# Optimization experiments

Measured on AMD Instinct MI355X. Metric: run time of the kernel, lower is better.

## Reference

```python
import jax, jax.numpy as jnp
import numpy as np

D_MODEL = 1024
NUM_HEADS = 16
D_K = D_MODEL // NUM_HEADS


def setup_inputs() -> dict:
    key = jax.random.key(0)
    ks = jax.random.split(key, 11)
    B, S = 4, 2048
    s = 1.0 / np.sqrt(D_MODEL)
    inp = {
        "q": jax.random.normal(ks[0], (B, S, D_MODEL), jnp.float32),
        "k": jax.random.normal(ks[1], (B, S, D_MODEL), jnp.float32),
        "v": jax.random.normal(ks[2], (B, S, D_MODEL), jnp.float32),
        "w_q": jax.random.normal(ks[3], (D_MODEL, D_MODEL), jnp.float32) * s,
        "b_q": jnp.zeros((D_MODEL,), jnp.float32),
        "w_k": jax.random.normal(ks[4], (D_MODEL, D_MODEL), jnp.float32) * s,
        "b_k": jnp.zeros((D_MODEL,), jnp.float32),
        "w_v": jax.random.normal(ks[5], (D_MODEL, D_MODEL), jnp.float32) * s,
        "b_v": jnp.zeros((D_MODEL,), jnp.float32),
        "w_o": jax.random.normal(ks[6], (D_MODEL, D_MODEL), jnp.float32) * s,
        "b_o": jnp.zeros((D_MODEL,), jnp.float32),
    }
    return inp


def reference(q, k, v, w_q, b_q, w_k, b_k, w_v, b_v, w_o, b_o):
    B, S, _ = q.shape
    # projections; weights stored as [in, out] so x @ W + b
    def proj(x, w, b):
        y = x @ w + b  # [B, S, d_model]
        return y.reshape(B, -1, NUM_HEADS, D_K).transpose(0, 2, 1, 3)  # [B,H,S,d_k]
    qh = proj(q, w_q, b_q)
    kh = proj(k, w_k, b_k)
    vh = proj(v, w_v, b_v)
    scores = jnp.einsum("bhsd,bhtd->bhst", qh, kh) / jnp.sqrt(jnp.float32(D_K))
    attn = jax.nn.softmax(scores, axis=-1)  # dropout p=0.0 -> identity
    x = jnp.einsum("bhst,bhtd->bhsd", attn, vh)
    x = x.transpose(0, 2, 1, 3).reshape(B, S, D_MODEL)
    return x @ w_o + b_o
```

## Files before the change

kernel.cpp:

```cpp
#include <hip/hip_runtime.h>
#include <hip/hip_bf16.h>
#include <stdint.h>

#define D_MODEL 1024
#define SEQ 2048
#define BATCH 4
#define NHEADS 16
#define ROWS (BATCH*SEQ)

#define QKSCALE 0.18033688011f

typedef __attribute__((ext_vector_type(4))) float f32x4;
typedef __attribute__((ext_vector_type(8))) short short8;
typedef __attribute__((ext_vector_type(4))) unsigned int uint4v;

#if __has_builtin(__builtin_amdgcn_exp2f)
#define EXP2(x) __builtin_amdgcn_exp2f(x)
#else
#define EXP2(x) exp2f(x)
#endif

__device__ __forceinline__ unsigned short f2bf(float f) {
    unsigned int x = __builtin_bit_cast(unsigned int, f);
    x += 0x7fffu + ((x >> 16) & 1u);
    return (unsigned short)(x >> 16);
}

__device__ __forceinline__ unsigned int cvtpk(float a, float b) {
    unsigned int r;
    asm("v_cvt_pk_bf16_f32 %0, %1, %2" : "=v"(r) : "v"(a), "v"(b));
    return r;
}

__global__ __launch_bounds__(256) void wtrans_kernel(const float* __restrict__ w0,
                                                     const float* __restrict__ w1,
                                                     const float* __restrict__ w2,
                                                     const float* __restrict__ w3,
                                                     unsigned short* __restrict__ wt0,
                                                     unsigned short* __restrict__ wt1,
                                                     unsigned short* __restrict__ wt2,
                                                     unsigned short* __restrict__ wt3) {
    const int z = blockIdx.z;
    const float* w = (z == 0) ? w0 : (z == 1) ? w1 : (z == 2) ? w2 : w3;
    unsigned short* wt = (z == 0) ? wt0 : (z == 1) ? wt1 : (z == 2) ? wt2 : wt3;
    __shared__ float tile[32][33];
    int tx = threadIdx.x & 31;
    int ty = threadIdx.x >> 5;
    int r0 = blockIdx.y * 32, c0 = blockIdx.x * 32;
    #pragma unroll
    for (int i = 0; i < 4; ++i)
        tile[ty + 8*i][tx] = w[(size_t)(r0 + ty + 8*i) * D_MODEL + (c0 + tx)];
    __syncthreads();
    int t = threadIdx.x;
    if (t < 128) {
        int n_loc = t >> 2;
        int kc = t & 3;
        int n = c0 + n_loc;
        int kbase = r0 + kc*8;
        uint4v pk;
        #pragma unroll
        for (int j = 0; j < 4; ++j)
            pk[j] = cvtpk(tile[kc*8 + 2*j][n_loc], tile[kc*8 + 2*j + 1][n_loc]);
        size_t tidx = (size_t)(n >> 7) * 16 + (kbase >> 6);
        int row = n & 127;
        int byte = (row*128 + (kbase & 63)*2) ^ ((row & 7) << 4);
        *(uint4v*)((char*)wt + tidx*16384 + byte) = pk;
    }
}

__global__ __launch_bounds__(256) void qkv_gemm_kernel(
        const float* __restrict__ qin, const float* __restrict__ kin,
        const float* __restrict__ vin,
        const unsigned short* __restrict__ wqt, const unsigned short* __restrict__ wkt,
        const unsigned short* __restrict__ wvt,
        const float* __restrict__ bq, const float* __restrict__ bk,
        const float* __restrict__ bv,
        unsigned short* __restrict__ qhd, unsigned short* __restrict__ khd,
        unsigned short* __restrict__ vtd) {
    __shared__ __attribute__((aligned(16))) unsigned short Alds[2][128*64];
    __shared__ __attribute__((aligned(16))) unsigned short Blds[2][128*64];
    const int z = blockIdx.z;
    const float* Af = (z == 0) ? qin : (z == 1) ? kin : vin;
    const unsigned short* Bt = (z == 0) ? wqt : (z == 1) ? wkt : wvt;
    const float* bias = (z == 0) ? bq : (z == 1) ? bk : bv;
    const int m0 = blockIdx.x * 128;
    const int n0 = blockIdx.y * 128;
    const int t = threadIdx.x;
    const int lane = t & 63;
    const int w = t >> 6;
    const int wm = w >> 1, wn = w & 1;
    const int l15 = lane & 15, lg = lane >> 4;

    f32x4 acc[4][4];
    #pragma unroll
    for (int i = 0; i < 4; ++i)
        #pragma unroll
        for (int j = 0; j < 4; ++j) acc[i][j] = (f32x4)(0.0f);

    #pragma unroll
    for (int i = 0; i < 8; ++i) {
        int idx = t + i*256;
        int row = idx >> 4, c4 = idx & 15;
        f32x4 v = *(const f32x4*)(Af + (size_t)(m0+row)*D_MODEL + c4*4);
        unsigned long long pk = (unsigned long long)cvtpk(v[0], v[1])
                              | ((unsigned long long)cvtpk(v[2], v[3]) << 32);
        int byte = (row*128 + c4*8) ^ ((row & 7) << 4);
        *(unsigned long long*)((char*)Alds[0] + byte) = pk;
    }
    {
        const unsigned short* tsrc = Bt + (size_t)(n0 >> 7) * 16 * 8192;
        #pragma unroll
        for (int i = 0; i < 4; ++i)
            __builtin_amdgcn_global_load_lds(
                (const __attribute__((address_space(1))) void*)(tsrc + t*8 + i*2048),
                (__attribute__((address_space(3))) void*)(Blds[0] + t*8 + i*2048),
                16, 0, 0);
    }
    __syncthreads();

    #pragma unroll 2
    for (int kt = 0; kt < 16; ++kt) {
        const int cur = kt & 1, nxt = cur ^ 1;
        const int k0n = (kt + 1) * 64;
        f32x4 av[8];
        if (kt < 15) {
            #pragma unroll
            for (int i = 0; i < 8; ++i) {
                int idx = t + i*256;
                int row = idx >> 4, c4 = idx & 15;
                av[i] = *(const f32x4*)(Af + (size_t)(m0+row)*D_MODEL + k0n + c4*4);
            }
            const unsigned short* tsrc = Bt + ((size_t)(n0 >> 7) * 16 + (k0n >> 6)) * 8192;
            #pragma unroll
            for (int i = 0; i < 4; ++i)
                __builtin_amdgcn_global_load_lds(
                    (const __attribute__((address_space(1))) void*)(tsrc + t*8 + i*2048),
                    (__attribute__((address_space(3))) void*)(Blds[nxt] + t*8 + i*2048),
                    16, 0, 0);
        }

        #pragma unroll
        for (int kk = 0; kk < 2; ++kk) {
            short8 af[4], bfr[4];
            #pragma unroll
            for (int mi = 0; mi < 4; ++mi) {
                int row = wm*64 + mi*16 + l15;
                int byte = (row*128 + kk*64 + lg*16) ^ ((row & 7) << 4);
                af[mi] = *(const short8*)((const char*)Alds[cur] + byte);
            }
            #pragma unroll
            for (int ni = 0; ni < 4; ++ni) {
                int row = wn*64 + ni*16 + l15;
                int byte = (row*128 + kk*64 + lg*16) ^ ((row & 7) << 4);
                bfr[ni] = *(const short8*)((const char*)Blds[cur] + byte);
            }
            #pragma unroll
            for (int mi = 0; mi < 4; ++mi)
                #pragma unroll
                for (int ni = 0; ni < 4; ++ni)
                    acc[mi][ni] = __builtin_amdgcn_mfma_f32_16x16x32_bf16(
                        af[mi], bfr[ni], acc[mi][ni], 0, 0, 0);
        }

        if (kt < 15) {
            #pragma unroll
            for (int i = 0; i < 8; ++i) {
                int idx = t + i*256;
                int row = idx >> 4, c4 = idx & 15;
                unsigned long long pk = (unsigned long long)cvtpk(av[i][0], av[i][1])
                                      | ((unsigned long long)cvtpk(av[i][2], av[i][3]) << 32);
                int byte = (row*128 + c4*8) ^ ((row & 7) << 4);
                *(unsigned long long*)((char*)Alds[nxt] + byte) = pk;
            }
        }
        __syncthreads();
    }

    #pragma unroll
    for (int mi = 0; mi < 4; ++mi)
        #pragma unroll
        for (int ni = 0; ni < 4; ++ni) {
            int col = n0 + wn*64 + ni*16 + l15;
            float bv_ = bias[col];
            int h = col >> 6, d = col & 63;
            if (z == 0) {
                #pragma unroll
                for (int r = 0; r < 4; ++r) {
                    int row = m0 + wm*64 + mi*16 + lg*4 + r;
                    int bb = row >> 11, s = row & 2047;
                    float vv = (acc[mi][ni][r] + bv_) * QKSCALE;
                    qhd[(((size_t)(bb*NHEADS + h)*SEQ + s) << 6) + d] = f2bf(vv);
                }
            } else if (z == 1) {
                #pragma unroll
                for (int r = 0; r < 4; ++r) {
                    int row = m0 + wm*64 + mi*16 + lg*4 + r;
                    int bb = row >> 11, s = row & 2047;
                    int ti = s >> 6, kvl = s & 63;
                    int ph = (kvl & 0x23) | ((kvl & 4) << 2) | ((kvl & 0x18) >> 1);
                    int byte = (ph*128 + d*2) ^ ((ph & 7) << 4);
                    *(unsigned short*)((char*)khd
                        + ((size_t)(bb*NHEADS + h)*32 + ti)*8192 + byte)
                        = f2bf(acc[mi][ni][r] + bv_);
                }
            } else {
                int row0 = m0 + wm*64 + mi*16 + lg*4;
                int bb = row0 >> 11, s0 = row0 & 2047;
                int ti = s0 >> 6, kvl0 = s0 & 63;
                unsigned long long pk = 0;
                #pragma unroll
                for (int r = 0; r < 4; ++r)
                    pk |= (unsigned long long)f2bf(acc[mi][ni][r] + bv_) << (16*r);
                int byte = (d*128 + kvl0*2) ^ ((d & 7) << 4);
                *(unsigned long long*)((char*)vtd
                    + ((size_t)(bb*NHEADS + h)*32 + ti)*8192 + byte) = pk;
            }
        }
}

__global__ __launch_bounds__(256) void out_gemm_kernel(const unsigned short* __restrict__ Ab,
                                                       const unsigned short* __restrict__ Bt,
                                                       const float* __restrict__ bias,
                                                       float* __restrict__ Out) {
    __shared__ __attribute__((aligned(16))) unsigned short Alds[2][128*64];
    __shared__ __attribute__((aligned(16))) unsigned short Blds[2][128*64];
    const int m0 = blockIdx.x * 128;
    const int n0 = blockIdx.y * 128;
    const int t = threadIdx.x;
    const int lane = t & 63;
    const int w = t >> 6;
    const int wm = w >> 1, wn = w & 1;
    const int l15 = lane & 15, lg = lane >> 4;

    const int arow = t >> 3;
    const int acb = ((t & 7) * 16) ^ ((arow & 7) << 4);

    f32x4 acc[4][4];
    #pragma unroll
    for (int i = 0; i < 4; ++i)
        #pragma unroll
        for (int j = 0; j < 4; ++j) acc[i][j] = (f32x4)(0.0f);

    #pragma unroll
    for (int i = 0; i < 4; ++i) {
        const char* src = (const char*)(Ab + (size_t)(m0 + arow + i*32)*D_MODEL) + acb;
        __builtin_amdgcn_global_load_lds(
            (const __attribute__((address_space(1))) void*)src,
            (__attribute__((address_space(3))) void*)(Alds[0] + t*8 + i*2048),
            16, 0, 0);
    }
    {
        const unsigned short* tsrc = Bt + (size_t)(n0 >> 7) * 16 * 8192;
        #pragma unroll
        for (int i = 0; i < 4; ++i)
            __builtin_amdgcn_global_load_lds(
                (const __attribute__((address_space(1))) void*)(tsrc + t*8 + i*2048),
                (__attribute__((address_space(3))) void*)(Blds[0] + t*8 + i*2048),
                16, 0, 0);
    }
    __syncthreads();

    #pragma unroll 2
    for (int kt = 0; kt < 16; ++kt) {
        const int cur = kt & 1, nxt = cur ^ 1;
        const int k0n = (kt + 1) * 64;
        if (kt < 15) {
            #pragma unroll
            for (int i = 0; i < 4; ++i) {
                const char* src = (const char*)(Ab + (size_t)(m0 + arow + i*32)*D_MODEL + k0n) + acb;
                __builtin_amdgcn_global_load_lds(
                    (const __attribute__((address_space(1))) void*)src,
                    (__attribute__((address_space(3))) void*)(Alds[nxt] + t*8 + i*2048),
                    16, 0, 0);
            }
            const unsigned short* tsrc = Bt + ((size_t)(n0 >> 7) * 16 + (k0n >> 6)) * 8192;
            #pragma unroll
            for (int i = 0; i < 4; ++i)
                __builtin_amdgcn_global_load_lds(
                    (const __attribute__((address_space(1))) void*)(tsrc + t*8 + i*2048),
                    (__attribute__((address_space(3))) void*)(Blds[nxt] + t*8 + i*2048),
                    16, 0, 0);
        }

        #pragma unroll
        for (int kk = 0; kk < 2; ++kk) {
            short8 af[4], bfr[4];
            #pragma unroll
            for (int mi = 0; mi < 4; ++mi) {
                int row = wm*64 + mi*16 + l15;
                int byte = (row*128 + kk*64 + lg*16) ^ ((row & 7) << 4);
                af[mi] = *(const short8*)((const char*)Alds[cur] + byte);
            }
            #pragma unroll
            for (int ni = 0; ni < 4; ++ni) {
                int row = wn*64 + ni*16 + l15;
                int byte = (row*128 + kk*64 + lg*16) ^ ((row & 7) << 4);
                bfr[ni] = *(const short8*)((const char*)Blds[cur] + byte);
            }
            #pragma unroll
            for (int mi = 0; mi < 4; ++mi)
                #pragma unroll
                for (int ni = 0; ni < 4; ++ni)
                    acc[mi][ni] = __builtin_amdgcn_mfma_f32_16x16x32_bf16(
                        af[mi], bfr[ni], acc[mi][ni], 0, 0, 0);
        }
        __syncthreads();
    }

    #pragma unroll
    for (int mi = 0; mi < 4; ++mi)
        #pragma unroll
        for (int ni = 0; ni < 4; ++ni) {
            int col = n0 + wn*64 + ni*16 + l15;
            float bv_ = bias[col];
            #pragma unroll
            for (int r = 0; r < 4; ++r) {
                int row = m0 + wm*64 + mi*16 + lg*4 + r;
                Out[(size_t)row*D_MODEL + col] = acc[mi][ni][r] + bv_;
            }
        }
}

__global__ __launch_bounds__(256, 4) void attn_kernel(const unsigned short* __restrict__ qh,
                                                      const unsigned short* __restrict__ kimg_all,
                                                      const unsigned short* __restrict__ vimg_all,
                                                      unsigned short* __restrict__ xout) {
    __shared__ __attribute__((aligned(16))) unsigned short Klds[2][64*64];
    __shared__ __attribute__((aligned(16))) unsigned short Vtl[2][64*64];

    const int bid = blockIdx.x;
    const int xcd = bid & 7, idx = bid >> 3;
    const int qb = idx >> 3;
    const int bh = ((idx & 7) << 3) | xcd;
    const int t = threadIdx.x;
    const int lane = t & 63;
    const int w = t >> 6;
    const int l15 = lane & 15, lg = lane >> 4;

    const unsigned short* qbase = qh + (size_t)bh * SEQ * 64;
    const unsigned short* kimg = kimg_all + (size_t)bh * SEQ * 64;
    const unsigned short* vimg = vimg_all + (size_t)bh * SEQ * 64;

    short8 qf[2][2];
    #pragma unroll
    for (int l = 0; l < 2; ++l) {
        int qrow = qb*128 + w*32 + l*16 + l15;
        qf[l][0] = *(const short8*)(qbase + (size_t)qrow*64 + lg*8);
        qf[l][1] = *(const short8*)(qbase + (size_t)qrow*64 + 32 + lg*8);
    }

    int fb[4][2];
    #pragma unroll
    for (int nb = 0; nb < 4; ++nb) {
        int rr = nb*16 + l15;
        int sw = (rr & 7) << 4;
        fb[nb][0] = (rr*128 + lg*16) ^ sw;
        fb[nb][1] = (rr*128 + 64 + lg*16) ^ sw;
    }

    float m[2] = {-1e30f, -1e30f};
    float lsum[2] = {0.f, 0.f};
    f32x4 o[2][4];
    #pragma unroll
    for (int l = 0; l < 2; ++l)
        #pragma unroll
        for (int nb = 0; nb < 4; ++nb) o[l][nb] = (f32x4)(0.0f);

    #pragma unroll
    for (int i = 0; i < 2; ++i) {
        __builtin_amdgcn_global_load_lds(
            (const __attribute__((address_space(1))) void*)(kimg + t*8 + i*2048),
            (__attribute__((address_space(3))) void*)(Klds[0] + t*8 + i*2048), 16, 0, 0);
        __builtin_amdgcn_global_load_lds(
            (const __attribute__((address_space(1))) void*)(vimg + t*8 + i*2048),
            (__attribute__((address_space(3))) void*)(Vtl[0] + t*8 + i*2048), 16, 0, 0);
    }
    __syncthreads();

    const unsigned short* kp = kimg + 4096 + t*8;
    const unsigned short* vp = vimg + 4096 + t*8;

    const int NT = SEQ/64;
    #pragma unroll 2
    for (int ti = 0; ti < NT; ++ti) {
        const int c = ti & 1;
        if (ti + 1 < NT) {
            #pragma unroll
            for (int i = 0; i < 2; ++i) {
                __builtin_amdgcn_global_load_lds(
                    (const __attribute__((address_space(1))) void*)(kp + i*2048),
                    (__attribute__((address_space(3))) void*)(Klds[c^1] + t*8 + i*2048), 16, 0, 0);
                __builtin_amdgcn_global_load_lds(
                    (const __attribute__((address_space(1))) void*)(vp + i*2048),
                    (__attribute__((address_space(3))) void*)(Vtl[c^1] + t*8 + i*2048), 16, 0, 0);
            }
            kp += 4096; vp += 4096;
        }
        const char* Kc = (const char*)Klds[c];
        const char* Vc = (const char*)Vtl[c];

        f32x4 s4[2][4];
        #pragma unroll
        for (int nb = 0; nb < 4; ++nb) {
            short8 kf0 = *(const short8*)(Kc + fb[nb][0]);
            short8 kf1 = *(const short8*)(Kc + fb[nb][1]);
            __builtin_amdgcn_s_setprio(1);
            #pragma unroll
            for (int l = 0; l < 2; ++l) {
                f32x4 s = (f32x4)(0.0f);
                s = __builtin_amdgcn_mfma_f32_16x16x32_bf16(kf0, qf[l][0], s, 0, 0, 0);
                s = __builtin_amdgcn_mfma_f32_16x16x32_bf16(kf1, qf[l][1], s, 0, 0, 0);
                s4[l][nb] = s;
            }
            __builtin_amdgcn_s_setprio(0);
        }

        if (ti == 0) {
            #pragma unroll
            for (int l = 0; l < 2; ++l) {
                float tm = s4[l][0][0];
                #pragma unroll
                for (int nb = 0; nb < 4; ++nb)
                    #pragma unroll
                    for (int r = 0; r < 4; ++r) tm = fmaxf(tm, s4[l][nb][r]);
                tm = fmaxf(tm, __shfl_xor(tm, 16));
                tm = fmaxf(tm, __shfl_xor(tm, 32));
                m[l] = tm;
            }
        }

        union U { short8 s; unsigned int u[4]; } pa[2][2];
        #pragma unroll
        for (int l = 0; l < 2; ++l) {
            float p[16];
            float ts = 0.f;
            #pragma unroll
            for (int nb = 0; nb < 4; ++nb)
                #pragma unroll
                for (int r = 0; r < 4; ++r) {
                    float pv = EXP2(s4[l][nb][r] - m[l]);
                    p[nb*4 + r] = pv;
                    ts += pv;
                }
            lsum[l] += ts;

            pa[l][0].u[0] = cvtpk(p[0],  p[1]);  pa[l][0].u[1] = cvtpk(p[2],  p[3]);
            pa[l][0].u[2] = cvtpk(p[4],  p[5]);  pa[l][0].u[3] = cvtpk(p[6],  p[7]);
            pa[l][1].u[0] = cvtpk(p[8],  p[9]);  pa[l][1].u[1] = cvtpk(p[10], p[11]);
            pa[l][1].u[2] = cvtpk(p[12], p[13]); pa[l][1].u[3] = cvtpk(p[14], p[15]);
        }

        #pragma unroll
        for (int nb = 0; nb < 4; ++nb) {
            short8 vf0 = *(const short8*)(Vc + fb[nb][0]);
            short8 vf1 = *(const short8*)(Vc + fb[nb][1]);
            __builtin_amdgcn_s_setprio(1);
            o[0][nb] = __builtin_amdgcn_mfma_f32_16x16x32_bf16(pa[0][0].s, vf0, o[0][nb], 0, 0, 0);
            o[0][nb] = __builtin_amdgcn_mfma_f32_16x16x32_bf16(pa[0][1].s, vf1, o[0][nb], 0, 0, 0);
            o[1][nb] = __builtin_amdgcn_mfma_f32_16x16x32_bf16(pa[1][0].s, vf0, o[1][nb], 0, 0, 0);
            o[1][nb] = __builtin_amdgcn_mfma_f32_16x16x32_bf16(pa[1][1].s, vf1, o[1][nb], 0, 0, 0);
            __builtin_amdgcn_s_setprio(0);
        }

        __syncthreads();
    }

    const int bb = bh >> 4, h = bh & 15;
    #pragma unroll
    for (int l = 0; l < 2; ++l) {
        float lt = lsum[l];
        lt += __shfl_xor(lt, 16);
        lt += __shfl_xor(lt, 32);
        float rl[4];
        #pragma unroll
        for (int r = 0; r < 4; ++r) rl[r] = 1.0f / __shfl(lt, lg*4 + r);
        #pragma unroll
        for (int nb = 0; nb < 4; ++nb)
            #pragma unroll
            for (int r = 0; r < 4; ++r) {
                int s = qb*128 + w*32 + l*16 + lg*4 + r;
                int d = nb*16 + l15;
                xout[((size_t)(bb*SEQ + s))*D_MODEL + h*64 + d] = f2bf(o[l][nb][r] * rl[r]);
            }
    }
}

extern "C" void kernel_launch(void* const* d_in, const int* in_sizes, int n_in,
                              void* d_out, int out_size, void* d_ws, size_t ws_size,
                              hipStream_t stream) {
    (void)in_sizes; (void)n_in; (void)out_size; (void)ws_size;
    const float* q  = (const float*)d_in[0];
    const float* k  = (const float*)d_in[1];
    const float* v  = (const float*)d_in[2];
    const float* wq = (const float*)d_in[3];
    const float* bq = (const float*)d_in[4];
    const float* wk = (const float*)d_in[5];
    const float* bk = (const float*)d_in[6];
    const float* wv = (const float*)d_in[7];
    const float* bv = (const float*)d_in[8];
    const float* wo = (const float*)d_in[9];
    const float* bo = (const float*)d_in[10];

    char* ws = (char*)d_ws;
    unsigned short* wqt = (unsigned short*)(ws);
    unsigned short* wkt = (unsigned short*)(ws + (2ull << 20));
    unsigned short* wvt = (unsigned short*)(ws + (4ull << 20));
    unsigned short* wot = (unsigned short*)(ws + (6ull << 20));
    unsigned short* qhd = (unsigned short*)(ws + (8ull << 20));
    unsigned short* khd = (unsigned short*)(ws + (24ull << 20));
    unsigned short* vtd = (unsigned short*)(ws + (40ull << 20));
    unsigned short* xat = (unsigned short*)(ws + (56ull << 20));

    hipLaunchKernelGGL(wtrans_kernel, dim3(D_MODEL/32, D_MODEL/32, 4), dim3(256), 0, stream,
                       wq, wk, wv, wo, wqt, wkt, wvt, wot);

    hipLaunchKernelGGL(qkv_gemm_kernel, dim3(ROWS/128, D_MODEL/128, 3), dim3(256), 0, stream,
                       q, k, v, wqt, wkt, wvt, bq, bk, bv, qhd, khd, vtd);

    hipLaunchKernelGGL(attn_kernel, dim3(16*64), dim3(256), 0, stream,
                       qhd, khd, vtd, xat);

    hipLaunchKernelGGL(out_gemm_kernel, dim3(ROWS/128, D_MODEL/128), dim3(256), 0, stream,
                       xat, wot, bo, (float*)d_out);
}
```

Baseline: 189.5 us.

## Triple-buffer B/K/V tiles with explicit vmcnt waits to prefetch two stages ahead

```diff
diff --git a/kernel.cpp b/kernel.cpp
--- a/kernel.cpp
+++ b/kernel.cpp
@@ -20,6 +20,14 @@
 #define EXP2(x) exp2f(x)
 #endif
 
+#define PIPE_SYNC(VM) do { \
+    __builtin_amdgcn_sched_barrier(0); \
+    asm volatile("s_waitcnt vmcnt(" VM ") lgkmcnt(0)" ::: "memory"); \
+    __builtin_amdgcn_sched_barrier(0); \
+    __builtin_amdgcn_s_barrier(); \
+    __builtin_amdgcn_sched_barrier(0); \
+} while (0)
+
 __device__ __forceinline__ unsigned short f2bf(float f) {
     unsigned int x = __builtin_bit_cast(unsigned int, f);
     x += 0x7fffu + ((x >> 16) & 1u);
@@ -30,6 +38,12 @@
     unsigned int r;
     asm("v_cvt_pk_bf16_f32 %0, %1, %2" : "=v"(r) : "v"(a), "v"(b));
     return r;
+}
+
+__device__ __forceinline__ void gload16(const unsigned short* src, unsigned short* dst) {
+    __builtin_amdgcn_global_load_lds(
+        (const __attribute__((address_space(1))) void*)src,
+        (__attribute__((address_space(3))) void*)dst, 16, 0, 0);
 }
 
 __global__ __launch_bounds__(256) void wtrans_kernel(const float* __restrict__ w0,
@@ -78,7 +92,7 @@
         unsigned short* __restrict__ qhd, unsigned short* __restrict__ khd,
         unsigned short* __restrict__ vtd) {
     __shared__ __attribute__((aligned(16))) unsigned short Alds[2][128*64];
-    __shared__ __attribute__((aligned(16))) unsigned short Blds[2][128*64];
+    __shared__ __attribute__((aligned(16))) unsigned short Blds[3][128*64];
     const int z = blockIdx.z;
     const float* Af = (z == 0) ? qin : (z == 1) ? kin : vin;
     const unsigned short* Bt = (z == 0) ? wqt : (z == 1) ? wkt : wvt;
@@ -90,6 +104,7 @@
     const int w = t >> 6;
     const int wm = w >> 1, wn = w & 1;
     const int l15 = lane & 15, lg = lane >> 4;
+    const unsigned short* tbase = Bt + (size_t)(n0 >> 7) * 16 * 8192;
 
     f32x4 acc[4][4];
     #pragma unroll
@@ -107,36 +122,31 @@
         int byte = (row*128 + c4*8) ^ ((row & 7) << 4);
         *(unsigned long long*)((char*)Alds[0] + byte) = pk;
     }
-    {
-        const unsigned short* tsrc = Bt + (size_t)(n0 >> 7) * 16 * 8192;
-        #pragma unroll
-        for (int i = 0; i < 4; ++i)
-            __builtin_amdgcn_global_load_lds(
-                (const __attribute__((address_space(1))) void*)(tsrc + t*8 + i*2048),
-                (__attribute__((address_space(3))) void*)(Blds[0] + t*8 + i*2048),
-                16, 0, 0);
-    }
-    __syncthreads();
-
-    #pragma unroll 2
+    #pragma unroll
+    for (int i = 0; i < 4; ++i) gload16(tbase + t*8 + i*2048, Blds[0] + t*8 + i*2048);
+    #pragma unroll
+    for (int i = 0; i < 4; ++i) gload16(tbase + 8192 + t*8 + i*2048, Blds[1] + t*8 + i*2048);
+    PIPE_SYNC("4");
+
+    int cbr = 0;
+    #pragma unroll 1
     for (int kt = 0; kt < 16; ++kt) {
-        const int cur = kt & 1, nxt = cur ^ 1;
-        const int k0n = (kt + 1) * 64;
+        const int ca = kt & 1, na = ca ^ 1;
         f32x4 av[8];
         if (kt < 15) {
+            const int k0n = (kt + 1) * 64;
             #pragma unroll
             for (int i = 0; i < 8; ++i) {
                 int idx = t + i*256;
                 int row = idx >> 4, c4 = idx & 15;
                 av[i] = *(const f32x4*)(Af + (size_t)(m0+row)*D_MODEL + k0n + c4*4);
             }
-            const unsigned short* tsrc = Bt + ((size_t)(n0 >> 7) * 16 + (k0n >> 6)) * 8192;
-            #pragma unroll
-            for (int i = 0; i < 4; ++i)
-                __builtin_amdgcn_global_load_lds(
-                    (const __attribute__((address_space(1))) void*)(tsrc + t*8 + i*2048),
-                    (__attribute__((address_space(3))) void*)(Blds[nxt] + t*8 + i*2048),
-                    16, 0, 0);
+        }
+        if (kt < 14) {
+            int cbw = cbr + 2; if (cbw >= 3) cbw -= 3;
+            const unsigned short* tsrc = tbase + (size_t)(kt + 2) * 8192;
+            #pragma unroll
+            for (int i = 0; i < 4; ++i) gload16(tsrc + t*8 + i*2048, Blds[cbw] + t*8 + i*2048);
         }
 
         #pragma unroll
@@ -146,13 +156,13 @@
             for (int mi = 0; mi < 4; ++mi) {
                 int row = wm*64 + mi*16 + l15;
                 int byte = (row*128 + kk*64 + lg*16) ^ ((row & 7) << 4);
-                af[mi] = *(const short8*)((const char*)Alds[cur] + byte);
+                af[mi] = *(const short8*)((const char*)Alds[ca] + byte);
             }
             #pragma unroll
             for (int ni = 0; ni < 4; ++ni) {
                 int row = wn*64 + ni*16 + l15;
                 int byte = (row*128 + kk*64 + lg*16) ^ ((row & 7) << 4);
-                bfr[ni] = *(const short8*)((const char*)Blds[cur] + byte);
+                bfr[ni] = *(const short8*)((const char*)Blds[cbr] + byte);
             }
             #pragma unroll
             for (int mi = 0; mi < 4; ++mi)
@@ -170,10 +180,12 @@
                 unsigned long long pk = (unsigned long long)cvtpk(av[i][0], av[i][1])
                                       | ((unsigned long long)cvtpk(av[i][2], av[i][3]) << 32);
                 int byte = (row*128 + c4*8) ^ ((row & 7) << 4);
-                *(unsigned long long*)((char*)Alds[nxt] + byte) = pk;
-            }
-        }
-        __syncthreads();
+                *(unsigned long long*)((char*)Alds[na] + byte) = pk;
+            }
+        }
+        if (kt < 14)       { PIPE_SYNC("4"); }
+        else if (kt == 14) { PIPE_SYNC("0"); }
+        cbr = (cbr == 2) ? 0 : cbr + 1;
     }
 
     #pragma unroll
@@ -223,7 +235,7 @@
                                                        const float* __restrict__ bias,
                                                        float* __restrict__ Out) {
     __shared__ __attribute__((aligned(16))) unsigned short Alds[2][128*64];
-    __shared__ __attribute__((aligned(16))) unsigned short Blds[2][128*64];
+    __shared__ __attribute__((aligned(16))) unsigned short Blds[3][128*64];
     const int m0 = blockIdx.x * 128;
     const int n0 = blockIdx.y * 128;
     const int t = threadIdx.x;
@@ -231,6 +243,7 @@
     const int w = t >> 6;
     const int wm = w >> 1, wn = w & 1;
     const int l15 = lane & 15, lg = lane >> 4;
+    const unsigned short* tbase = Bt + (size_t)(n0 >> 7) * 16 * 8192;
 
     const int arow = t >> 3;
     const int acb = ((t & 7) * 16) ^ ((arow & 7) << 4);
@@ -244,42 +257,31 @@
     #pragma unroll
     for (int i = 0; i < 4; ++i) {
         const char* src = (const char*)(Ab + (size_t)(m0 + arow + i*32)*D_MODEL) + acb;
-        __builtin_amdgcn_global_load_lds(
-            (const __attribute__((address_space(1))) void*)src,
-            (__attribute__((address_space(3))) void*)(Alds[0] + t*8 + i*2048),
-            16, 0, 0);
-    }
-    {
-        const unsigned short* tsrc = Bt + (size_t)(n0 >> 7) * 16 * 8192;
-        #pragma unroll
-        for (int i = 0; i < 4; ++i)
-            __builtin_amdgcn_global_load_lds(
-                (const __attribute__((address_space(1))) void*)(tsrc + t*8 + i*2048),
-                (__attribute__((address_space(3))) void*)(Blds[0] + t*8 + i*2048),
-                16, 0, 0);
-    }
-    __syncthreads();
-
-    #pragma unroll 2
+        gload16((const unsigned short*)src, Alds[0] + t*8 + i*2048);
+    }
+    #pragma unroll
+    for (int i = 0; i < 4; ++i) gload16(tbase + t*8 + i*2048, Blds[0] + t*8 + i*2048);
+    #pragma unroll
+    for (int i = 0; i < 4; ++i) gload16(tbase + 8192 + t*8 + i*2048, Blds[1] + t*8 + i*2048);
+    PIPE_SYNC("4");
+
+    int cbr = 0;
+    #pragma unroll 1
     for (int kt = 0; kt < 16; ++kt) {
-        const int cur = kt & 1, nxt = cur ^ 1;
-        const int k0n = (kt + 1) * 64;
+        const int ca = kt & 1, na = ca ^ 1;
         if (kt < 15) {
+            const int k0n = (kt + 1) * 64;
             #pragma unroll
             for (int i = 0; i < 4; ++i) {
                 const char* src = (const char*)(Ab + (size_t)(m0 + arow + i*32)*D_MODEL + k0n) + acb;
-                __builtin_amdgcn_global_load_lds(
-                    (const __attribute__((address_space(1))) void*)src,
-                    (__attribute__((address_space(3))) void*)(Alds[nxt] + t*8 + i*2048),
-                    16, 0, 0);
-            }
-            const unsigned short* tsrc = Bt + ((size_t)(n0 >> 7) * 16 + (k0n >> 6)) * 8192;
-            #pragma unroll
-            for (int i = 0; i < 4; ++i)
-                __builtin_amdgcn_global_load_lds(
-                    (const __attribute__((address_space(1))) void*)(tsrc + t*8 + i*2048),
-                    (__attribute__((address_space(3))) void*)(Blds[nxt] + t*8 + i*2048),
-                    16, 0, 0);
+                gload16((const unsigned short*)src, Alds[na] + t*8 + i*2048);
+            }
+        }
+        if (kt < 14) {
+            int cbw = cbr + 2; if (cbw >= 3) cbw -= 3;
+            const unsigned short* tsrc = tbase + (size_t)(kt + 2) * 8192;
+            #pragma unroll
+            for (int i = 0; i < 4; ++i) gload16(tsrc + t*8 + i*2048, Blds[cbw] + t*8 + i*2048);
         }
 
         #pragma unroll
@@ -289,13 +291,13 @@
             for (int mi = 0; mi < 4; ++mi) {
                 int row = wm*64 + mi*16 + l15;
                 int byte = (row*128 + kk*64 + lg*16) ^ ((row & 7) << 4);
-                af[mi] = *(const short8*)((const char*)Alds[cur] + byte);
+                af[mi] = *(const short8*)((const char*)Alds[ca] + byte);
             }
             #pragma unroll
             for (int ni = 0; ni < 4; ++ni) {
                 int row = wn*64 + ni*16 + l15;
                 int byte = (row*128 + kk*64 + lg*16) ^ ((row & 7) << 4);
-                bfr[ni] = *(const short8*)((const char*)Blds[cur] + byte);
+                bfr[ni] = *(const short8*)((const char*)Blds[cbr] + byte);
             }
             #pragma unroll
             for (int mi = 0; mi < 4; ++mi)
@@ -304,7 +306,9 @@
                     acc[mi][ni] = __builtin_amdgcn_mfma_f32_16x16x32_bf16(
                         af[mi], bfr[ni], acc[mi][ni], 0, 0, 0);
         }
-        __syncthreads();
+        if (kt < 14)       { PIPE_SYNC("4"); }
+        else if (kt == 14) { PIPE_SYNC("0"); }
+        cbr = (cbr == 2) ? 0 : cbr + 1;
     }
 
     #pragma unroll
@@ -325,8 +329,8 @@
                                                       const unsigned short* __restrict__ kimg_all,
                                                       const unsigned short* __restrict__ vimg_all,
                                                       unsigned short* __restrict__ xout) {
-    __shared__ __attribute__((aligned(16))) unsigned short Klds[2][64*64];
-    __shared__ __attribute__((aligned(16))) unsigned short Vtl[2][64*64];
+    __shared__ __attribute__((aligned(16))) unsigned short Klds[3][64*64];
+    __shared__ __attribute__((aligned(16))) unsigned short Vtl[3][64*64];
 
     const int bid = blockIdx.x;
     const int xcd = bid & 7, idx = bid >> 3;
@@ -367,37 +371,33 @@
         for (int nb = 0; nb < 4; ++nb) o[l][nb] = (f32x4)(0.0f);
 
     #pragma unroll
-    for (int i = 0; i < 2; ++i) {
-        __builtin_amdgcn_global_load_lds(
-            (const __attribute__((address_space(1))) void*)(kimg + t*8 + i*2048),
-            (__attribute__((address_space(3))) void*)(Klds[0] + t*8 + i*2048), 16, 0, 0);
-        __builtin_amdgcn_global_load_lds(
-            (const __attribute__((address_space(1))) void*)(vimg + t*8 + i*2048),
-            (__attribute__((address_space(3))) void*)(Vtl[0] + t*8 + i*2048), 16, 0, 0);
-    }
-    __syncthreads();
-
-    const unsigned short* kp = kimg + 4096 + t*8;
-    const unsigned short* vp = vimg + 4096 + t*8;
+    for (int j = 0; j < 2; ++j) {
+        const unsigned short* ks = kimg + (size_t)j*4096 + t*8;
+        const unsigned short* vs = vimg + (size_t)j*4096 + t*8;
+        #pragma unroll
+        for (int i = 0; i < 2; ++i) {
+            gload16(ks + i*2048, Klds[j] + t*8 + i*2048);
+            gload16(vs + i*2048, Vtl[j] + t*8 + i*2048);
+        }
+    }
+    PIPE_SYNC("4");
 
     const int NT = SEQ/64;
-    #pragma unroll 2
+    int cr = 0;
+    #pragma unroll 1
     for (int ti = 0; ti < NT; ++ti) {
-        const int c = ti & 1;
-        if (ti + 1 < NT) {
+        if (ti < NT - 2) {
+            int cw = cr + 2; if (cw >= 3) cw -= 3;
+            const unsigned short* ks = kimg + (size_t)(ti + 2)*4096 + t*8;
+            const unsigned short* vs = vimg + (size_t)(ti + 2)*4096 + t*8;
             #pragma unroll
             for (int i = 0; i < 2; ++i) {
-                __builtin_amdgcn_global_load_lds(
-                    (const __attribute__((address_space(1))) void*)(kp + i*2048),
-                    (__attribute__((address_space(3))) void*)(Klds[c^1] + t*8 + i*2048), 16, 0, 0);
-                __builtin_amdgcn_global_load_lds(
-                    (const __attribute__((address_space(1))) void*)(vp + i*2048),
-                    (__attribute__((address_space(3))) void*)(Vtl[c^1] + t*8 + i*2048), 16, 0, 0);
-            }
-            kp += 4096; vp += 4096;
-        }
-        const char* Kc = (const char*)Klds[c];
-        const char* Vc = (const char*)Vtl[c];
+                gload16(ks + i*2048, Klds[cw] + t*8 + i*2048);
+                gload16(vs + i*2048, Vtl[cw] + t*8 + i*2048);
+            }
+        }
+        const char* Kc = (const char*)Klds[cr];
+        const char* Vc = (const char*)Vtl[cr];
 
         f32x4 s4[2][4];
         #pragma unroll
@@ -462,7 +462,9 @@
             __builtin_amdgcn_s_setprio(0);
         }
 
-        __syncthreads();
+        if (ti < NT - 2)       { PIPE_SYNC("4"); }
+        else if (ti == NT - 2) { PIPE_SYNC("0"); }
+        cr = (cr == 2) ? 0 : cr + 1;
     }
 
     const int bb = bh >> 4, h = bh & 15;
```

Measured after the change: 223.1 us. +17.7%, slower.
